# Performance work log

Measured on AMD Instinct MI355X. Metric: run time of the kernel, lower is better.

Reference implementation:

```python
import jax, jax.numpy as jnp
import numpy as np

N_NODES = 50000
N_EDGES = 800000
N_LABEL = 200000
FEAT = 128
HID = 32
HEADS = 8
NEG_SLOPE = 0.2


def gat_conv(x, edge_index, w_src, w_dst, att_src, att_dst, bias, heads):
    """PyG GATConv with add_self_loops=False, concat=True, dropout=0.
    x: [N, F_in]; edge_index: [2, E] (row 0 = source j, row 1 = target i).
    w_src/w_dst: [F_in, heads*C]; att_src/att_dst: [heads, C]; bias: [heads*C].
    """
    N = x.shape[0]
    C = w_src.shape[1] // heads
    xs = (x @ w_src).reshape(N, heads, C)  # source-side projection
    xd = (x @ w_dst).reshape(N, heads, C)  # target-side projection
    a_s = (xs * att_src[None]).sum(-1)     # [N, H]
    a_d = (xd * att_dst[None]).sum(-1)     # [N, H]
    src, dst = edge_index[0], edge_index[1]
    alpha = jax.nn.leaky_relu(a_s[src] + a_d[dst], NEG_SLOPE)  # [E, H]
    # softmax over incoming edges of each target node
    m = jax.ops.segment_max(alpha, dst, num_segments=N)
    m = jnp.where(jnp.isfinite(m), m, 0.0)
    e = jnp.exp(alpha - m[dst])
    denom = jax.ops.segment_sum(e, dst, num_segments=N)
    coef = e / (denom[dst] + 1e-16)        # [E, H]
    msg = xs[src] * coef[:, :, None]       # [E, H, C]
    out = jax.ops.segment_sum(msg, dst, num_segments=N)  # [N, H, C]
    return out.reshape(N, heads * C) + bias


def setup_inputs() -> dict:
    key = jax.random.key(0)
    ks = jax.random.split(key, 16)
    H1 = HEADS * HID  # 256

    def w(k, fan_in, shape):
        return jax.random.normal(k, shape, dtype=jnp.float32) / np.sqrt(fan_in)

    return {
        "x": jax.random.normal(ks[0], (N_NODES, FEAT), dtype=jnp.float32),
        "edge_index": jax.random.randint(ks[1], (2, N_EDGES), 0, N_NODES),
        "edge_label_index": jax.random.randint(ks[2], (2, N_LABEL), 0, N_NODES),
        # node_lin: Linear(FEAT, HID)
        "lin_w": w(ks[3], FEAT, (FEAT, HID)),
        "lin_b": jnp.zeros((HID,), dtype=jnp.float32),
        # conv1: GATConv(HID -> HID, heads=8)
        "w1s": w(ks[4], HID, (HID, H1)),
        "w1d": w(ks[5], HID, (HID, H1)),
        "a1s": w(ks[6], HID, (HEADS, HID)),
        "a1d": w(ks[7], HID, (HEADS, HID)),
        "b1": jnp.zeros((H1,), dtype=jnp.float32),
        # conv2: GATConv(H1 -> HID, heads=1)
        "w2s": w(ks[8], H1, (H1, HID)),
        "w2d": w(ks[9], H1, (H1, HID)),
        "a2s": w(ks[10], HID, (1, HID)),
        "a2d": w(ks[11], HID, (1, HID)),
        "b2": jnp.zeros((HID,), dtype=jnp.float32),
    }


def reference(x, edge_index, edge_label_index, lin_w, lin_b,
              w1s, w1d, a1s, a1d, b1, w2s, w2d, a2s, a2d, b2):
    h = x @ lin_w + lin_b                                   # [N, HID]
    h = jax.nn.relu(gat_conv(h, edge_index, w1s, w1d, a1s, a1d, b1, HEADS))  # [N, H*C]
    h = gat_conv(h, edge_index, w2s, w2d, a2s, a2d, b2, 1)  # [N, HID]
    # Classifier: dot product of endpoint embeddings
    pred = (h[edge_label_index[0]] * h[edge_label_index[1]]).sum(-1)  # [N_LABEL]
    return pred
```

## Files before the change

### kernel.cpp

```cpp
#include <hip/hip_runtime.h>

#define NN 50000
#define NE 800000
#define NL 200000
#define FEAT 128
#define HID 32
#define HEADS 8
#define H1 256
#define CAP 64
#define NB 32

using u32 = unsigned int;

__device__ __forceinline__ float bflo(u32 v) { return __uint_as_float(v << 16); }
__device__ __forceinline__ float bfhi(u32 v) { return __uint_as_float(v & 0xffff0000u); }
__device__ __forceinline__ u32 packbf(float a, float b) {
  u32 ua = __float_as_uint(a), ub = __float_as_uint(b);
  ua += 0x7fffu + ((ua >> 16) & 1u);
  ub += 0x7fffu + ((ub >> 16) & 1u);
  return (ua >> 16) | (ub & 0xffff0000u);
}

__global__ __launch_bounds__(256) void k_vprep(
    const float* __restrict__ w1s, const float* __restrict__ w1d,
    const float* __restrict__ a1s, const float* __restrict__ a1d,
    const float* __restrict__ w2s, const float* __restrict__ w2d,
    const float* __restrict__ a2s, const float* __restrict__ a2d,
    float* __restrict__ v1s, float* __restrict__ v1d,
    float* __restrict__ v2s, float* __restrict__ v2d) {
  int tid = threadIdx.x;
  int k = tid >> 3, h = tid & 7;
  float ss = 0.f, sd = 0.f;
  for (int c = 0; c < 32; ++c) {
    ss += w1s[k * H1 + h * 32 + c] * a1s[h * 32 + c];
    sd += w1d[k * H1 + h * 32 + c] * a1d[h * 32 + c];
  }
  v1s[k * 8 + h] = ss;
  v1d[k * 8 + h] = sd;
  float s2 = 0.f, d2 = 0.f;
  for (int c = 0; c < 32; ++c) {
    s2 += w2s[tid * 32 + c] * a2s[c];
    d2 += w2d[tid * 32 + c] * a2d[c];
  }
  v2s[tid] = s2;
  v2d[tid] = d2;
}

__global__ void k_fill(const int* __restrict__ src, const int* __restrict__ dst,
                       int* __restrict__ cnt, int* __restrict__ csr) {
  int e = blockIdx.x * 256 + threadIdx.x;
  if (e >= NE) return;
  int d = dst[e];
  int slot = atomicAdd(&cnt[d], 1);
  if (slot < CAP) csr[(size_t)d * CAP + slot] = src[e];
}

__global__ __launch_bounds__(256) void k_l1(
    const float* __restrict__ x, const float* __restrict__ lin_w,
    const float* __restrict__ lin_b, const float* __restrict__ v1s,
    const float* __restrict__ v1d, u32* __restrict__ h0b,
    float* __restrict__ as1, float* __restrict__ ad1) {
  __shared__ float wl[FEAT * HID];
  __shared__ float xl[32 * FEAT];
  __shared__ float h0l[32 * HID];
  __shared__ float vsl[HID * 8], vdl[HID * 8], bl[HID];
  int tid = threadIdx.x;
  for (int i = tid; i < (FEAT * HID) / 4; i += 256)
    ((float4*)wl)[i] = ((const float4*)lin_w)[i];
  vsl[tid] = v1s[tid];
  vdl[tid] = v1d[tid];
  if (tid < HID) bl[tid] = lin_b[tid];
  int n0 = blockIdx.x * 32;
  for (int i = tid; i < (32 * FEAT) / 4; i += 256) {
    int n = n0 + (i >> 5);
    ((float4*)xl)[i] = (n < NN) ? ((const float4*)x)[(size_t)n * 32 + (i & 31)]
                                : make_float4(0.f, 0.f, 0.f, 0.f);
  }
  __syncthreads();
  {
    int nl = tid >> 5, c = tid & 31;
    float acc[4] = {0.f, 0.f, 0.f, 0.f};
    for (int k = 0; k < FEAT; ++k) {
      float wv = wl[k * HID + c];
#pragma unroll
      for (int j = 0; j < 4; ++j) acc[j] += xl[(nl + 8 * j) * FEAT + k] * wv;
    }
#pragma unroll
    for (int j = 0; j < 4; ++j) h0l[(nl + 8 * j) * HID + c] = acc[j] + bl[c];
  }
  __syncthreads();
  for (int i = tid; i < 512; i += 256) {
    int nl = i >> 4, cp = i & 15;
    int n = n0 + nl;
    if (n < NN)
      h0b[(size_t)n * 16 + cp] =
          packbf(h0l[nl * 32 + 2 * cp], h0l[nl * 32 + 2 * cp + 1]);
  }
  {
    int nl = tid >> 3, h = tid & 7;
    int n = n0 + nl;
    if (n < NN) {
      float ss = 0.f, sd = 0.f;
#pragma unroll
      for (int k = 0; k < HID; ++k) {
        float hv = h0l[nl * HID + k];
        ss += hv * vsl[k * 8 + h];
        sd += hv * vdl[k * 8 + h];
      }
      as1[(size_t)n * 8 + h] = ss;
      ad1[(size_t)n * 8 + h] = sd;
    }
  }
}

__global__ __launch_bounds__(256) void k_aggE(
    const int* __restrict__ cnt, const int* __restrict__ csr,
    const u32* __restrict__ h0b, const float* __restrict__ as1,
    const float* __restrict__ ad1, u32* __restrict__ aggb,
    float* __restrict__ den1) {
  int tid = threadIdx.x;
  int w = tid >> 6, lane = tid & 63;
  int half = lane >> 5, c = lane & 31;
  int n = blockIdx.x * 4 + w;
  int hh = c;
  bool ise = hh < 8;
  float adreg = ise ? ad1[(size_t)n * 8 + hh] : 0.f;
  float acc[8] = {0.f, 0.f, 0.f, 0.f, 0.f, 0.f, 0.f, 0.f};
  float den = 0.f;
  int m = min(cnt[n], CAP);
  const int* cs = csr + (size_t)n * CAP;
  int sb = lane & 32;
  int cp = c >> 1;
  int j = 0;
  for (; j + 3 < m; j += 4) {
    int s0 = cs[j + half];
    int s1 = cs[j + 2 + half];
    u32 w0 = h0b[(size_t)s0 * 16 + cp];
    u32 w1 = h0b[(size_t)s1 * 16 + cp];
    float e0 = 0.f, e1 = 0.f;
    if (ise) {
      float a0 = as1[(size_t)s0 * 8 + hh] + adreg;
      a0 = a0 > 0.f ? a0 : 0.2f * a0;
      float a1 = as1[(size_t)s1 * 8 + hh] + adreg;
      a1 = a1 > 0.f ? a1 : 0.2f * a1;
      e0 = __expf(a0);
      e1 = __expf(a1);
      den += e0 + e1;
    }
    float h0v = (c & 1) ? bfhi(w0) : bflo(w0);
    float h1v = (c & 1) ? bfhi(w1) : bflo(w1);
#pragma unroll
    for (int h = 0; h < 8; ++h)
      acc[h] += __shfl(e0, sb + h) * h0v + __shfl(e1, sb + h) * h1v;
  }
  for (; j < m; j += 2) {
    int idx = j + half;
    int sA = cs[idx < m ? idx : m - 1];
    u32 wv = h0b[(size_t)sA * 16 + cp];
    float e = 0.f;
    if (ise && idx < m) {
      float a = as1[(size_t)sA * 8 + hh] + adreg;
      a = a > 0.f ? a : 0.2f * a;
      e = __expf(a);
      den += e;
    }
    float hv = (c & 1) ? bfhi(wv) : bflo(wv);
#pragma unroll
    for (int h = 0; h < 8; ++h) acc[h] += __shfl(e, sb + h) * hv;
  }
#pragma unroll
  for (int h = 0; h < 8; ++h) acc[h] += __shfl_xor(acc[h], 32);
  den += __shfl_xor(den, 32);
  if (lane < 8) den1[(size_t)n * 8 + lane] = den;
#pragma unroll
  for (int h = 0; h < 8; ++h) {
    float other = __shfl_xor(acc[h], 1);
    if (lane < 32 && !(lane & 1))
      aggb[(size_t)n * 128 + h * 16 + cp] = packbf(acc[h], other);
  }
}

__global__ __launch_bounds__(256) void k_p12(
    const u32* __restrict__ aggb, const float* __restrict__ den1,
    const float* __restrict__ w1s, const float* __restrict__ b1,
    const float* __restrict__ w2s, const float* __restrict__ v2s,
    const float* __restrict__ v2d, u32* __restrict__ xs2b,
    float* __restrict__ as2, float* __restrict__ ad2) {
  __shared__ u32 aggl[NB * 128];
  __shared__ float sh1[NB * 257];
  __shared__ float denl[NB * 8];
  __shared__ float v2sl[H1], v2dl[H1];
  int tid = threadIdx.x;
  int n0 = blockIdx.x * NB;
  int h = tid >> 5, c = tid & 31;
  float w1reg[32], w2reg[32];
#pragma unroll
  for (int k = 0; k < 32; ++k) w1reg[k] = w1s[k * H1 + tid];
#pragma unroll
  for (int k = 0; k < 32; ++k) w2reg[k] = w2s[h * 1024 + k * 32 + c];
  float b1reg = b1[tid];
  v2sl[tid] = v2s[tid];
  v2dl[tid] = v2d[tid];
  for (int q = 0; q < 4; ++q) {
    int i = tid + 256 * q;
    int nn = n0 + (i >> 5);
    ((uint4*)aggl)[i] = (nn < NN) ? ((const uint4*)aggb)[(size_t)n0 * 32 + i]
                                  : make_uint4(0u, 0u, 0u, 0u);
  }
  {
    int nn = n0 + (tid >> 3);
    denl[tid] = (nn < NN) ? den1[(size_t)nn * 8 + (tid & 7)] : 1.f;
  }
  __syncthreads();
  for (int n = 0; n < NB; ++n) {
    float out = 0.f;
#pragma unroll
    for (int kp = 0; kp < 16; ++kp) {
      u32 v = aggl[n * 128 + h * 16 + kp];
      out += bflo(v) * w1reg[2 * kp] + bfhi(v) * w1reg[2 * kp + 1];
    }
    float inv = 1.f / (denl[n * 8 + h] + 1e-16f);
    float r = out * inv + b1reg;
    sh1[n * 257 + tid] = r > 0.f ? r : 0.f;
  }
  __syncthreads();
  float* part = (float*)aggl;
  int wv = tid >> 6, lane = tid & 63;
  for (int n = 0; n < NB; ++n) {
    float pp = 0.f;
#pragma unroll
    for (int k = 0; k < 32; ++k)
      pp += sh1[n * 257 + h * 32 + k] * w2reg[k];
    pp += __shfl_xor(pp, 32);
    if (lane < 32) part[wv * (NB * 32) + n * 32 + c] = pp;
  }
  __syncthreads();
#pragma unroll
  for (int q = 0; q < 4; ++q) {
    int slot = tid + 256 * q;
    int nn = slot >> 5, cc = slot & 31;
    float s = part[slot] + part[1024 + slot] + part[2048 + slot] +
              part[3072 + slot];
    float other = __shfl_xor(s, 1);
    int gn = n0 + nn;
    if (gn < NN && !(cc & 1))
      xs2b[(size_t)gn * 16 + (cc >> 1)] = packbf(s, other);
  }
  {
    int nn = tid >> 3, kg = tid & 7;
    float ssum = 0.f, dsum = 0.f;
#pragma unroll
    for (int k = 0; k < 32; ++k) {
      int ki = kg * 32 + ((k + 4 * kg) & 31);
      float hv = sh1[nn * 257 + ki];
      ssum += hv * v2sl[ki];
      dsum += hv * v2dl[ki];
    }
    ssum += __shfl_xor(ssum, 1);
    dsum += __shfl_xor(dsum, 1);
    ssum += __shfl_xor(ssum, 2);
    dsum += __shfl_xor(dsum, 2);
    ssum += __shfl_xor(ssum, 4);
    dsum += __shfl_xor(dsum, 4);
    int gn = n0 + nn;
    if (kg == 0 && gn < NN) {
      as2[gn] = ssum;
      ad2[gn] = dsum;
    }
  }
}

__global__ __launch_bounds__(256) void k_agg2(
    const int* __restrict__ cnt, const int* __restrict__ csr,
    const u32* __restrict__ xs2b, const float* __restrict__ as2,
    const float* __restrict__ ad2, const float* __restrict__ b2,
    float* __restrict__ h2) {
  int tid = threadIdx.x;
  int n = blockIdx.x * 8 + (tid >> 5);
  int sub = tid & 31, g = sub >> 4, l = sub & 15;
  if (n >= NN) return;
  float adn = ad2[n];
  int m = min(cnt[n], CAP);
  const int* cs = csr + (size_t)n * CAP;
  float a0 = 0.f, a1v = 0.f, ea = 0.f;
  int j = g;
  for (; j + 2 < m; j += 4) {
    int sA = cs[j], sB = cs[j + 2];
    float alA = as2[sA] + adn; alA = alA > 0.f ? alA : 0.2f * alA;
    float alB = as2[sB] + adn; alB = alB > 0.f ? alB : 0.2f * alB;
    float eA = __expf(alA), eB = __expf(alB);
    u32 vA = xs2b[(size_t)sA * 16 + l], vB = xs2b[(size_t)sB * 16 + l];
    a0 += bflo(vA) * eA + bflo(vB) * eB;
    a1v += bfhi(vA) * eA + bfhi(vB) * eB;
    ea += eA + eB;
  }
  for (; j < m; j += 2) {
    int s = cs[j];
    float al = as2[s] + adn; al = al > 0.f ? al : 0.2f * al;
    float ee = __expf(al);
    u32 v = xs2b[(size_t)s * 16 + l];
    a0 += bflo(v) * ee;
    a1v += bfhi(v) * ee;
    ea += ee;
  }
  a0 += __shfl_xor(a0, 16);
  a1v += __shfl_xor(a1v, 16);
  ea += __shfl_xor(ea, 16);
  if (g == 0) {
    float inv = 1.f / (ea + 1e-16f);
    float o0 = a0 * inv + b2[2 * l];
    float o1 = a1v * inv + b2[2 * l + 1];
    ((float2*)h2)[(size_t)n * 16 + l] = make_float2(o0, o1);
  }
}

__global__ __launch_bounds__(256) void k_pred(const int* __restrict__ eli,
                                              const float* __restrict__ h2,
                                              float* __restrict__ out) {
  int gid = blockIdx.x * 256 + threadIdx.x;
  int lab = gid >> 3, q = gid & 7;
  if (lab >= NL) return;
  int a = eli[lab], b = eli[NL + lab];
  float4 va = ((const float4*)(h2 + (size_t)a * HID))[q];
  float4 vb = ((const float4*)(h2 + (size_t)b * HID))[q];
  float s = va.x * vb.x + va.y * vb.y + va.z * vb.z + va.w * vb.w;
  s += __shfl_xor(s, 1);
  s += __shfl_xor(s, 2);
  s += __shfl_xor(s, 4);
  if (q == 0) out[lab] = s;
}

extern "C" void kernel_launch(void* const* d_in, const int* in_sizes, int n_in,
                              void* d_out, int out_size, void* d_ws, size_t ws_size,
                              hipStream_t stream) {
  const float* x     = (const float*)d_in[0];
  const int*   ei    = (const int*)d_in[1];
  const int*   eli   = (const int*)d_in[2];
  const float* lin_w = (const float*)d_in[3];
  const float* lin_b = (const float*)d_in[4];
  const float* w1s   = (const float*)d_in[5];
  const float* w1d   = (const float*)d_in[6];
  const float* a1s   = (const float*)d_in[7];
  const float* a1d   = (const float*)d_in[8];
  const float* b1    = (const float*)d_in[9];
  const float* w2s   = (const float*)d_in[10];
  const float* w2d   = (const float*)d_in[11];
  const float* a2s   = (const float*)d_in[12];
  const float* a2d   = (const float*)d_in[13];
  const float* b2    = (const float*)d_in[14];
  float* out = (float*)d_out;

  char* p = (char*)d_ws;
  auto take = [&](size_t bytes) {
    char* r = p;
    p += (bytes + 255) & ~(size_t)255;
    return r;
  };
  int*   cnt  = (int*)take((size_t)NN * 4);
  int*   csr  = (int*)take((size_t)NN * CAP * 4);
  u32*   h0b  = (u32*)take((size_t)NN * 16 * 4);
  float* as1  = (float*)take((size_t)NN * 8 * 4);
  float* ad1  = (float*)take((size_t)NN * 8 * 4);
  u32*   aggb = (u32*)take((size_t)NN * 128 * 4);
  float* den1 = (float*)take((size_t)NN * 8 * 4);
  u32*   xs2b = (u32*)take((size_t)NN * 16 * 4);
  float* as2  = (float*)take((size_t)NN * 4);
  float* ad2  = (float*)take((size_t)NN * 4);
  float* h2   = (float*)take((size_t)NN * HID * 4);
  float* v1s  = (float*)take(256 * 4);
  float* v1d  = (float*)take(256 * 4);
  float* v2s  = (float*)take(256 * 4);
  float* v2d  = (float*)take(256 * 4);

  const int* esrc = ei;
  const int* edst = ei + NE;

  hipMemsetAsync(cnt, 0, (size_t)NN * 4, stream);
  k_vprep<<<1, 256, 0, stream>>>(w1s, w1d, a1s, a1d, w2s, w2d, a2s, a2d,
                                 v1s, v1d, v2s, v2d);
  k_fill<<<(NE + 255) / 256, 256, 0, stream>>>(esrc, edst, cnt, csr);
  k_l1<<<(NN + 31) / 32, 256, 0, stream>>>(x, lin_w, lin_b, v1s, v1d,
                                           h0b, as1, ad1);
  k_aggE<<<NN / 4, 256, 0, stream>>>(cnt, csr, h0b, as1, ad1, aggb, den1);
  k_p12<<<(NN + NB - 1) / NB, 256, 0, stream>>>(aggb, den1, w1s, b1, w2s,
                                                v2s, v2d, xs2b, as2, ad2);
  k_agg2<<<(NN + 7) / 8, 256, 0, stream>>>(cnt, csr, xs2b, as2, ad2, b2, h2);
  k_pred<<<(NL * 8 + 255) / 256, 256, 0, stream>>>(eli, h2, out);
}
```

Before: 300.3 us.

## Remap edge aggregation lanes per head and store layer-1 hidden as bf16

The edge aggregation kernel now maps each lane to a (head, 4-channel) slot, so every lane computes its own attention exponent and loads a uint2 of features. This removes the per-edge shuffle broadcast of eight head coefficients and the final cross-half reduction. In the projection kernel the layer-1 hidden activations are kept in shared memory as packed bf16, which halves LDS footprint and traffic. The inner dot products are split into four independent accumulators for more ILP. The cost is redundant exp computation across the 8 lanes of each head and extra bf16 rounding of the hidden activations.

```diff
diff --git a/kernel.cpp b/kernel.cpp
--- a/kernel.cpp
+++ b/kernel.cpp
@@ -120,64 +120,44 @@
     float* __restrict__ den1) {
   int tid = threadIdx.x;
   int w = tid >> 6, lane = tid & 63;
-  int half = lane >> 5, c = lane & 31;
+  int h = lane >> 3, cq = lane & 7;
   int n = blockIdx.x * 4 + w;
-  int hh = c;
-  bool ise = hh < 8;
-  float adreg = ise ? ad1[(size_t)n * 8 + hh] : 0.f;
-  float acc[8] = {0.f, 0.f, 0.f, 0.f, 0.f, 0.f, 0.f, 0.f};
-  float den = 0.f;
+  const uint2* h0b2 = (const uint2*)h0b;
+  float adreg = ad1[(size_t)n * 8 + h];
+  float a0 = 0.f, a1 = 0.f, a2 = 0.f, a3 = 0.f, den = 0.f;
   int m = min(cnt[n], CAP);
   const int* cs = csr + (size_t)n * CAP;
-  int sb = lane & 32;
-  int cp = c >> 1;
   int j = 0;
-  for (; j + 3 < m; j += 4) {
-    int s0 = cs[j + half];
-    int s1 = cs[j + 2 + half];
-    u32 w0 = h0b[(size_t)s0 * 16 + cp];
-    u32 w1 = h0b[(size_t)s1 * 16 + cp];
-    float e0 = 0.f, e1 = 0.f;
-    if (ise) {
-      float a0 = as1[(size_t)s0 * 8 + hh] + adreg;
-      a0 = a0 > 0.f ? a0 : 0.2f * a0;
-      float a1 = as1[(size_t)s1 * 8 + hh] + adreg;
-      a1 = a1 > 0.f ? a1 : 0.2f * a1;
-      e0 = __expf(a0);
-      e1 = __expf(a1);
-      den += e0 + e1;
-    }
-    float h0v = (c & 1) ? bfhi(w0) : bflo(w0);
-    float h1v = (c & 1) ? bfhi(w1) : bflo(w1);
-#pragma unroll
-    for (int h = 0; h < 8; ++h)
-      acc[h] += __shfl(e0, sb + h) * h0v + __shfl(e1, sb + h) * h1v;
-  }
-  for (; j < m; j += 2) {
-    int idx = j + half;
-    int sA = cs[idx < m ? idx : m - 1];
-    u32 wv = h0b[(size_t)sA * 16 + cp];
-    float e = 0.f;
-    if (ise && idx < m) {
-      float a = as1[(size_t)sA * 8 + hh] + adreg;
-      a = a > 0.f ? a : 0.2f * a;
-      e = __expf(a);
-      den += e;
-    }
-    float hv = (c & 1) ? bfhi(wv) : bflo(wv);
-#pragma unroll
-    for (int h = 0; h < 8; ++h) acc[h] += __shfl(e, sb + h) * hv;
-  }
-#pragma unroll
-  for (int h = 0; h < 8; ++h) acc[h] += __shfl_xor(acc[h], 32);
-  den += __shfl_xor(den, 32);
-  if (lane < 8) den1[(size_t)n * 8 + lane] = den;
-#pragma unroll
-  for (int h = 0; h < 8; ++h) {
-    float other = __shfl_xor(acc[h], 1);
-    if (lane < 32 && !(lane & 1))
-      aggb[(size_t)n * 128 + h * 16 + cp] = packbf(acc[h], other);
-  }
+  for (; j + 1 < m; j += 2) {
+    int sA = cs[j], sB = cs[j + 1];
+    float aA = as1[(size_t)sA * 8 + h] + adreg;
+    aA = aA > 0.f ? aA : 0.2f * aA;
+    float aB = as1[(size_t)sB * 8 + h] + adreg;
+    aB = aB > 0.f ? aB : 0.2f * aB;
+    float eA = __expf(aA), eB = __expf(aB);
+    uint2 wA = h0b2[(size_t)sA * 8 + cq];
+    uint2 wB = h0b2[(size_t)sB * 8 + cq];
+    den += eA + eB;
+    a0 += eA * bflo(wA.x) + eB * bflo(wB.x);
+    a1 += eA * bfhi(wA.x) + eB * bfhi(wB.x);
+    a2 += eA * bflo(wA.y) + eB * bflo(wB.y);
+    a3 += eA * bfhi(wA.y) + eB * bfhi(wB.y);
+  }
+  if (j < m) {
+    int sA = cs[j];
+    float aA = as1[(size_t)sA * 8 + h] + adreg;
+    aA = aA > 0.f ? aA : 0.2f * aA;
+    float eA = __expf(aA);
+    uint2 wA = h0b2[(size_t)sA * 8 + cq];
+    den += eA;
+    a0 += eA * bflo(wA.x);
+    a1 += eA * bfhi(wA.x);
+    a2 += eA * bflo(wA.y);
+    a3 += eA * bfhi(wA.y);
+  }
+  if (cq == 0) den1[(size_t)n * 8 + h] = den;
+  ((uint2*)aggb)[(size_t)n * 64 + h * 8 + cq] =
+      make_uint2(packbf(a0, a1), packbf(a2, a3));
 }
 
 __global__ __launch_bounds__(256) void k_p12(
@@ -187,7 +167,7 @@
     const float* __restrict__ v2d, u32* __restrict__ xs2b,
     float* __restrict__ as2, float* __restrict__ ad2) {
   __shared__ u32 aggl[NB * 128];
-  __shared__ float sh1[NB * 257];
+  __shared__ u32 sh1b[NB * 130];
   __shared__ float denl[NB * 8];
   __shared__ float v2sl[H1], v2dl[H1];
   int tid = threadIdx.x;
@@ -213,24 +193,38 @@
   }
   __syncthreads();
   for (int n = 0; n < NB; ++n) {
-    float out = 0.f;
-#pragma unroll
-    for (int kp = 0; kp < 16; ++kp) {
-      u32 v = aggl[n * 128 + h * 16 + kp];
-      out += bflo(v) * w1reg[2 * kp] + bfhi(v) * w1reg[2 * kp + 1];
-    }
+    const u32* ag = &aggl[n * 128 + h * 16];
+    float o0 = 0.f, o1 = 0.f, o2 = 0.f, o3 = 0.f;
+#pragma unroll
+    for (int kp = 0; kp < 4; ++kp) {
+      u32 v0 = ag[kp], v1 = ag[kp + 4], v2v = ag[kp + 8], v3 = ag[kp + 12];
+      o0 += bflo(v0) * w1reg[2 * kp] + bfhi(v0) * w1reg[2 * kp + 1];
+      o1 += bflo(v1) * w1reg[2 * kp + 8] + bfhi(v1) * w1reg[2 * kp + 9];
+      o2 += bflo(v2v) * w1reg[2 * kp + 16] + bfhi(v2v) * w1reg[2 * kp + 17];
+      o3 += bflo(v3) * w1reg[2 * kp + 24] + bfhi(v3) * w1reg[2 * kp + 25];
+    }
+    float out = (o0 + o1) + (o2 + o3);
     float inv = 1.f / (denl[n * 8 + h] + 1e-16f);
     float r = out * inv + b1reg;
-    sh1[n * 257 + tid] = r > 0.f ? r : 0.f;
+    r = r > 0.f ? r : 0.f;
+    float other = __shfl_xor(r, 1);
+    if (!(c & 1)) sh1b[n * 130 + h * 16 + (c >> 1)] = packbf(r, other);
   }
   __syncthreads();
   float* part = (float*)aggl;
   int wv = tid >> 6, lane = tid & 63;
   for (int n = 0; n < NB; ++n) {
-    float pp = 0.f;
-#pragma unroll
-    for (int k = 0; k < 32; ++k)
-      pp += sh1[n * 257 + h * 32 + k] * w2reg[k];
+    const u32* hp = &sh1b[n * 130 + h * 16];
+    float p0 = 0.f, p1 = 0.f, p2 = 0.f, p3 = 0.f;
+#pragma unroll
+    for (int kp = 0; kp < 4; ++kp) {
+      u32 v0 = hp[kp], v1 = hp[kp + 4], v2v = hp[kp + 8], v3 = hp[kp + 12];
+      p0 += bflo(v0) * w2reg[2 * kp] + bfhi(v0) * w2reg[2 * kp + 1];
+      p1 += bflo(v1) * w2reg[2 * kp + 8] + bfhi(v1) * w2reg[2 * kp + 9];
+      p2 += bflo(v2v) * w2reg[2 * kp + 16] + bfhi(v2v) * w2reg[2 * kp + 17];
+      p3 += bflo(v3) * w2reg[2 * kp + 24] + bfhi(v3) * w2reg[2 * kp + 25];
+    }
+    float pp = (p0 + p1) + (p2 + p3);
     pp += __shfl_xor(pp, 32);
     if (lane < 32) part[wv * (NB * 32) + n * 32 + c] = pp;
   }
@@ -250,11 +244,12 @@
     int nn = tid >> 3, kg = tid & 7;
     float ssum = 0.f, dsum = 0.f;
 #pragma unroll
-    for (int k = 0; k < 32; ++k) {
-      int ki = kg * 32 + ((k + 4 * kg) & 31);
-      float hv = sh1[nn * 257 + ki];
-      ssum += hv * v2sl[ki];
-      dsum += hv * v2dl[ki];
+    for (int q = 0; q < 16; ++q) {
+      int qq = (q + 2 * kg) & 15;
+      u32 v = sh1b[nn * 130 + kg * 16 + qq];
+      int ki = kg * 32 + 2 * qq;
+      ssum += bflo(v) * v2sl[ki] + bfhi(v) * v2sl[ki + 1];
+      dsum += bflo(v) * v2dl[ki] + bfhi(v) * v2dl[ki + 1];
     }
     ssum += __shfl_xor(ssum, 1);
     dsum += __shfl_xor(dsum, 1);
```

Result: slower. 318.3 us (+6.0%).
